# Kernel tuning notes

Hardware: AMD Instinct MI355X
Metric: run time of the kernel (lower is better)

Reference implementation:

```python
import jax, jax.numpy as jnp
import numpy as np

B, T, S, H = 32, 512, 1024, 512


def setup_inputs() -> dict:
    key = jax.random.key(0)
    k1, k2, k3, k4, k5, k6 = jax.random.split(key, 6)
    scale = 1.0 / np.sqrt(H)
    return {
        "query": jax.random.normal(k1, (B, T, H), dtype=jnp.float32),
        "encoder_outputs": jax.random.normal(k2, (B, S, H), dtype=jnp.float32),
        "src_lengths": jax.random.randint(k3, (B,), 1, S + 1, dtype=jnp.int32),
        "Ws": jax.random.normal(k4, (H, H), dtype=jnp.float32) * scale,  # torch Linear weight [out,in]
        "Wh": jax.random.normal(k5, (H, H), dtype=jnp.float32) * scale,
        "v": jax.random.normal(k6, (H,), dtype=jnp.float32) * scale,
    }


def reference(query, encoder_outputs, src_lengths, Ws, Wh, v):
    # score(h_s, q_t) = v^T tanh(Wh h_s + Ws q_t); masked softmax over src; weighted sum.
    S_ = encoder_outputs.shape[1]
    # Wh(encoder_outputs) computed once (loop in original recomputes it each step; same math).
    Whe = jnp.einsum('bsh,oh->bso', encoder_outputs, Wh)  # [B,S,H]
    mask = jnp.arange(S_)[None, :] < src_lengths[:, None]  # [B,S] valid positions

    def step(carry, q_t):  # q_t: [B,H]
        Wsq = jnp.einsum('bh,oh->bo', q_t, Ws)            # [B,H]
        scores = jnp.einsum('bsh,h->bs', jnp.tanh(Whe + Wsq[:, None, :]), v)  # [B,S]
        scores = jnp.where(mask, scores, -jnp.inf)
        attn = jax.nn.softmax(scores, axis=-1)            # [B,S]
        ctx = jnp.einsum('bs,bsh->bh', attn, encoder_outputs)  # [B,H]
        return carry, (ctx, attn)

    _, (ctx_t, attn_t) = jax.lax.scan(step, None, jnp.swapaxes(query, 0, 1))
    context_vectors = jnp.swapaxes(ctx_t, 0, 1)  # [B,T,H]
    # original returns attention weights from the LAST timestep only
    return context_vectors, attn_t[-1]
```

## Files before the change

### kernel.cpp

```cpp
#include <hip/hip_runtime.h>


constexpr int B = 32, T = 512, S = 1024, H = 512;
constexpr int TT = 16;
constexpr float C2LOG2E = 2.88539008177792681f;

typedef float vf4 __attribute__((ext_vector_type(4)));
typedef float f32x4 __attribute__((ext_vector_type(4)));
typedef short bf16x8 __attribute__((ext_vector_type(8)));
typedef unsigned short ushort_t;

#define DEVI __device__ __forceinline__

DEVI unsigned pack_bf16(float a, float b) {
  unsigned ua = __builtin_bit_cast(unsigned, a) + 0x8000u;
  unsigned ub = __builtin_bit_cast(unsigned, b) + 0x8000u;
  return (ub & 0xffff0000u) | (ua >> 16);
}
DEVI ushort_t to_bf16u(float x) {
  return (ushort_t)((__builtin_bit_cast(unsigned, x) + 0x8000u) >> 16);
}
DEVI float bf_lo(unsigned d) { return __builtin_bit_cast(float, d << 16); }
DEVI float bf_hi(unsigned d) { return __builtin_bit_cast(float, d & 0xffff0000u); }
DEVI float bf_one(ushort_t u) { return __builtin_bit_cast(float, (unsigned)u << 16); }
DEVI float exp2c(float x) {
  return __builtin_amdgcn_exp2f(fminf(fmaxf(x, -15.f), 15.f));
}

constexpr int QBLK = (B * T / 128) * 4;
constexpr int EBLK = (B * S / 128) * 4;

__global__ __launch_bounds__(256)
void mfma_matmul_kernel(const float* __restrict__ query, const float* __restrict__ enc,
                        const float* __restrict__ Ws, const float* __restrict__ Wh,
                        float* __restrict__ q4, float* __restrict__ e4,
                        const int* __restrict__ lens) {
  __shared__ short As[128][72];
  __shared__ short Bs[128][72];
  const int tid = threadIdx.x;
  int blk = blockIdx.x;
  const bool isE = blk >= QBLK;
  if (isE) blk -= QBLK;
  const int bx = blk & 3, by = blk >> 2;
  const int row0 = by * 128, col0 = bx * 128;
  const float* A = isE ? enc : query;
  const float* W = isE ? Wh : Ws;
  if (isE && (row0 % S) >= lens[row0 / S]) return;

  const int lr = tid >> 4;
  const int lc = (tid & 15) * 4;
  const int lane = tid & 63, wv = tid >> 6;
  const int wm = (wv >> 1) * 64, wn = (wv & 1) * 64;
  const int lrow = lane & 15, lkg = (lane >> 4) * 8;

  f32x4 acc[4][4] = {};
  for (int k0 = 0; k0 < H; k0 += 64) {
    __syncthreads();
#pragma unroll
    for (int u = 0; u < 8; ++u) {
      int r = lr + u * 16;
      float4 av = *(const float4*)&A[(size_t)(row0 + r) * H + k0 + lc];
      *(uint2*)&As[r][lc] = make_uint2(pack_bf16(av.x, av.y), pack_bf16(av.z, av.w));
      float4 wv4 = *(const float4*)&W[(size_t)(col0 + r) * H + k0 + lc];
      *(uint2*)&Bs[r][lc] = make_uint2(pack_bf16(wv4.x, wv4.y), pack_bf16(wv4.z, wv4.w));
    }
    __syncthreads();
#pragma unroll
    for (int ks = 0; ks < 64; ks += 32) {
      bf16x8 af[4], bfr[4];
#pragma unroll
      for (int i = 0; i < 4; ++i) {
        af[i] = *(const bf16x8*)&As[wm + i * 16 + lrow][ks + lkg];
        bfr[i] = *(const bf16x8*)&Bs[wn + i * 16 + lrow][ks + lkg];
      }
#pragma unroll
      for (int mt = 0; mt < 4; ++mt)
#pragma unroll
        for (int nt = 0; nt < 4; ++nt)
          acc[mt][nt] = __builtin_amdgcn_mfma_f32_16x16x32_bf16(
              af[mt], bfr[nt], acc[mt][nt], 0, 0, 0);
    }
  }

  const int crow = (lane >> 4) * 4, ccol = lane & 15;
  if (!isE) {
    const int b = row0 / T;
#pragma unroll
    for (int mt = 0; mt < 4; ++mt) {
      const int m = (row0 % T) + wm + mt * 16 + crow;
      const int tile_t = m >> 2;
#pragma unroll
      for (int nt = 0; nt < 4; ++nt) {
        const int n = col0 + wn + nt * 16 + ccol;
        float* base = q4 + (size_t)b * T * H + (size_t)tile_t * (4 * H) +
                      (n >> 2) * 16 + (n & 3);
        f32x4 a = acc[mt][nt];
#pragma unroll
        for (int reg = 0; reg < 4; ++reg) base[reg * 4] = exp2c(C2LOG2E * a[reg]);
      }
    }
  } else {
    const int b = row0 / S;
#pragma unroll
    for (int mt = 0; mt < 4; ++mt) {
      const int s0 = (row0 % S) + wm + mt * 16 + crow;
#pragma unroll
      for (int nt = 0; nt < 4; ++nt) {
        const int n = col0 + wn + nt * 16 + ccol;
        float* base = e4 + (size_t)b * H * S + (size_t)(n >> 2) * (4 * S) +
                      (size_t)s0 * 4 + (n & 3);
        f32x4 a = acc[mt][nt];
#pragma unroll
        for (int reg = 0; reg < 4; ++reg) base[reg * 4] = exp2c(C2LOG2E * a[reg]);
      }
    }
  }
}

DEVI void tree4(float& acc, vf4 q, vf4 vv, vf4 e) {
  float a0 = __builtin_fmaf(q[0], e[0], 1.0f);
  float a1 = __builtin_fmaf(q[1], e[1], 1.0f);
  float a2 = __builtin_fmaf(q[2], e[2], 1.0f);
  float a3 = __builtin_fmaf(q[3], e[3], 1.0f);
  float d01 = a0 * a1, d23 = a2 * a3;
  float n01 = __builtin_fmaf(vv[1], a0, vv[0] * a1);
  float n23 = __builtin_fmaf(vv[3], a2, vv[2] * a3);
  float d = d01 * d23;
  float n = __builtin_fmaf(n23, d01, n01 * d23);
  acc = __builtin_fmaf(n, __builtin_amdgcn_rcpf(d), acc);
}

DEVI vf4 qload(const ushort_t (&s_q16)[H / 4][64], int h4, int t) {
  uint2 qu = *(const uint2*)&s_q16[h4][t * 4];
  vf4 q = {bf_lo(qu.x), bf_hi(qu.x), bf_lo(qu.y), bf_hi(qu.y)};
  return q;
}

template <int NSIM>
DEVI void passN16(const ushort_t (&s_q16)[H / 4][64], const float* __restrict__ v,
                  const float* __restrict__ e4b, ushort_t (&s_sc16)[TT][S],
                  int wv, int lane) {
  float acc[NSIM][TT];
#pragma unroll
  for (int r = 0; r < NSIM; ++r)
#pragma unroll
    for (int t = 0; t < TT; ++t) acc[r][t] = 0.f;
  const float* ep = e4b + (size_t)(wv * 64 + lane) * 4;
  for (int h4 = 0; h4 < H / 4; ++h4) {
    vf4 e[NSIM];
#pragma unroll
    for (int r = 0; r < NSIM; ++r)
      e[r] = *(const vf4*)(ep + (size_t)h4 * (S * 4) + r * 1024);
    vf4 vv = *(const vf4*)(v + h4 * 4);
#pragma unroll
    for (int t = 0; t < TT; ++t) {
      vf4 q = qload(s_q16, h4, t);
#pragma unroll
      for (int r = 0; r < NSIM; ++r) tree4(acc[r][t], q, vv, e[r]);
    }
  }
#pragma unroll
  for (int r = 0; r < NSIM; ++r) {
    const int s = (wv + 4 * r) * 64 + lane;
#pragma unroll
    for (int t = 0; t < TT; ++t) s_sc16[t][s] = to_bf16u(-2.0f * acc[r][t]);
  }
}

template <int R>
DEVI void passTail16(const ushort_t (&s_q16)[H / 4][64], const float* __restrict__ v,
                     const float* __restrict__ e4b, ushort_t (&s_sc16)[TT][S],
                     int kbase, int wv, int lane) {
  float acc[R][4];
#pragma unroll
  for (int r = 0; r < R; ++r)
#pragma unroll
    for (int jj = 0; jj < 4; ++jj) acc[r][jj] = 0.f;
  const float* ep = e4b + (size_t)(kbase * 64 + lane) * 4;
  for (int h4 = 0; h4 < H / 4; ++h4) {
    vf4 vv = *(const vf4*)(v + h4 * 4);
    vf4 e[R];
#pragma unroll
    for (int r = 0; r < R; ++r)
      e[r] = *(const vf4*)(ep + (size_t)h4 * (S * 4) + r * 256);
#pragma unroll
    for (int jj = 0; jj < 4; ++jj) {
      vf4 q = qload(s_q16, h4, wv + 4 * jj);
#pragma unroll
      for (int r = 0; r < R; ++r) tree4(acc[r][jj], q, vv, e[r]);
    }
  }
#pragma unroll
  for (int r = 0; r < R; ++r)
#pragma unroll
    for (int jj = 0; jj < 4; ++jj)
      s_sc16[wv + 4 * jj][(kbase + r) * 64 + lane] = to_bf16u(-2.0f * acc[r][jj]);
}

__global__ __launch_bounds__(256, 3)
void attn_fused_kernel(const float* __restrict__ wsq, const float* __restrict__ wheT,
                       const float* __restrict__ enc, const float* __restrict__ v,
                       const int* __restrict__ lens, float* __restrict__ out) {
  __shared__ __align__(16) ushort_t s_sc16[TT][S];
  __shared__ __align__(16) ushort_t s_q16[H / 4][64];
  __shared__ float s_rs[TT];
  __shared__ long long s_w[32];
  __shared__ int s_bsel;

  const int tid = threadIdx.x;
  const int xcd = blockIdx.x & 7;
  const int j = blockIdx.x >> 3;
  const int slot = j >> 5;
  const int tt = j & 31;

  if (tid < 32) s_w[tid] = ((long long)lens[tid] << 8) + tid;
  __syncthreads();
  if (tid < 32) {
    long long wb = s_w[tid];
    int rank = 0;
#pragma unroll
    for (int b2 = 0; b2 < 32; ++b2) rank += (s_w[b2] > wb);
    int myrank = slot * 8 + ((slot & 1) ? (7 - xcd) : xcd);
    if (rank == myrank) s_bsel = tid;
  }
  __syncthreads();
  const int b = __builtin_amdgcn_readfirstlane(s_bsel);
  const int len = lens[b];

  {
    const vf4* src = (const vf4*)(wsq + (size_t)b * T * H + (size_t)tt * (TT * H));
    uint2* dst = (uint2*)&s_q16[0][0];
#pragma unroll
    for (int u = 0; u < 8; ++u) {
      int g = tid + u * 256;
      vf4 qv = src[g];
      int tile = g >> 9, rem = g & 511;
      int h4 = rem >> 2, i = rem & 3;
      uint2 pk = make_uint2(pack_bf16(qv[0], qv[1]), pack_bf16(qv[2], qv[3]));
      dst[h4 * 16 + tile * 4 + i] = pk;
    }
  }
  __syncthreads();

  {
    const int wv = tid >> 6, lane = tid & 63;
    const int NS = (len + 63) >> 6;
    const int nsw = NS >> 2;
    const int R = NS & 3;
    const float* e4b = wheT + (size_t)b * H * S;
    switch (nsw) {
      case 1: passN16<1>(s_q16, v, e4b, s_sc16, wv, lane); break;
      case 2: passN16<2>(s_q16, v, e4b, s_sc16, wv, lane); break;
      case 3: passN16<3>(s_q16, v, e4b, s_sc16, wv, lane); break;
      case 4: passN16<4>(s_q16, v, e4b, s_sc16, wv, lane); break;
      default: break;
    }
    switch (R) {
      case 1: passTail16<1>(s_q16, v, e4b, s_sc16, nsw * 4, wv, lane); break;
      case 2: passTail16<2>(s_q16, v, e4b, s_sc16, nsw * 4, wv, lane); break;
      case 3: passTail16<3>(s_q16, v, e4b, s_sc16, nsw * 4, wv, lane); break;
      default: break;
    }
  }
  __syncthreads();

  {
    const int wv = tid >> 6, lane = tid & 63;
#pragma unroll
    for (int jj = 0; jj < 4; ++jj) {
      const int tr = wv + 4 * jj;
      float vals[S / 64], ps[S / 64];
      float m = -3.0e38f;
#pragma unroll
      for (int i = 0; i < S / 64; ++i) {
        int s = lane + 64 * i;
        vals[i] = bf_one(s_sc16[tr][s]);
        if (s < len) m = fmaxf(m, vals[i]);
      }
#pragma unroll
      for (int o = 1; o < 64; o <<= 1) m = fmaxf(m, __shfl_xor(m, o, 64));
      float sum = 0.f;
#pragma unroll
      for (int i = 0; i < S / 64; ++i) {
        int s = lane + 64 * i;
        float p = (s < len) ? __builtin_amdgcn_exp2f((vals[i] - m) * 1.44269504088896341f) : 0.f;
        ps[i] = p;
        sum += p;
      }
#pragma unroll
      for (int o = 1; o < 64; o <<= 1) sum += __shfl_xor(sum, o, 64);
      float rs = 1.0f / sum;
#pragma unroll
      for (int i = 0; i < S / 64; ++i) s_sc16[tr][lane + 64 * i] = to_bf16u(ps[i]);
      if (lane == 0) s_rs[tr] = rs;
      if (tt == T / TT - 1 && tr == TT - 1) {
#pragma unroll
        for (int i = 0; i < S / 64; ++i)
          out[(size_t)B * T * H + (size_t)b * S + lane + 64 * i] = ps[i] * rs;
      }
    }
  }
  __syncthreads();

  {
    const int wv = tid >> 6, lane = tid & 63;
    const int h0 = lane * 4, h1 = 256 + lane * 4;
    float acc[4][8] = {};
    const float* encb = enc + (size_t)b * S * H;
    const int len4 = (len + 3) & ~3;
    for (int s0 = 0; s0 < len4; s0 += 4) {
      vf4 pr[4];
#pragma unroll
      for (int jj = 0; jj < 4; ++jj) {
        uint2 pu = *(const uint2*)&s_sc16[wv + 4 * jj][s0];
        pr[jj] = (vf4){bf_lo(pu.x), bf_hi(pu.x), bf_lo(pu.y), bf_hi(pu.y)};
      }
#pragma unroll
      for (int kk = 0; kk < 4; ++kk) {
        const float* er = encb + (size_t)(s0 + kk) * H;
        float4 e0 = *(const float4*)(er + h0);
        float4 e1 = *(const float4*)(er + h1);
        float ev[8] = {e0.x, e0.y, e0.z, e0.w, e1.x, e1.y, e1.z, e1.w};
#pragma unroll
        for (int jj = 0; jj < 4; ++jj)
#pragma unroll
          for (int q = 0; q < 8; ++q)
            acc[jj][q] = __builtin_fmaf(pr[jj][kk], ev[q], acc[jj][q]);
      }
    }
#pragma unroll
    for (int jj = 0; jj < 4; ++jj) {
      const int tr = wv + 4 * jj;
      const float rs = s_rs[tr];
      const size_t base = ((size_t)b * T + tt * TT + tr) * H;
      float4 o;
      o = make_float4(acc[jj][0] * rs, acc[jj][1] * rs, acc[jj][2] * rs, acc[jj][3] * rs);
      *(float4*)&out[base + h0] = o;
      o = make_float4(acc[jj][4] * rs, acc[jj][5] * rs, acc[jj][6] * rs, acc[jj][7] * rs);
      *(float4*)&out[base + h1] = o;
    }
  }
}

extern "C" void kernel_launch(void* const* d_in, const int* in_sizes, int n_in,
                              void* d_out, int out_size, void* d_ws, size_t ws_size,
                              hipStream_t stream) {
  const float* query = (const float*)d_in[0];
  const float* enc   = (const float*)d_in[1];
  const int*   lens  = (const int*)d_in[2];
  const float* Ws    = (const float*)d_in[3];
  const float* Wh    = (const float*)d_in[4];
  const float* v     = (const float*)d_in[5];
  float* out = (float*)d_out;
  float* wsq  = (float*)d_ws;
  float* wheT = wsq + (size_t)B * T * H;

  mfma_matmul_kernel<<<dim3(QBLK + EBLK), 256, 0, stream>>>(query, enc, Ws, Wh, wsq, wheT, lens);
  attn_fused_kernel<<<dim3(B * (T / TT)), 256, 0, stream>>>(wsq, wheT, enc, v, lens, out);
}
```

Before: 563.7 us.

## Stage bf16 query tile in quarters to shrink LDS and raise occupancy

Instead of converting the whole 16-timestep Wsq tile (512 hidden dims) into a 16 KB LDS buffer up front, the kernel now stages one quarter of the hidden dimension at a time into a 4 KB buffer inside the score passes, reloading from global for each quarter. This cuts LDS per block so more blocks can be resident, and launch bounds are raised from 3 to 4 waves-per-SIMD blocks. The cost is extra __syncthreads per quarter, re-staging the query for both main and tail passes, and tighter register limits that may cause spills for the larger NSIM variants.

```diff
diff --git a/kernel.cpp b/kernel.cpp
--- a/kernel.cpp
+++ b/kernel.cpp
@@ -130,33 +130,53 @@
   acc = __builtin_fmaf(n, __builtin_amdgcn_rcpf(d), acc);
 }
 
-DEVI vf4 qload(const ushort_t (&s_q16)[H / 4][64], int h4, int t) {
-  uint2 qu = *(const uint2*)&s_q16[h4][t * 4];
+DEVI vf4 qload4(const ushort_t (&s_q4)[32][64], int h4q, int t) {
+  uint2 qu = *(const uint2*)&s_q4[h4q][t * 4];
   vf4 q = {bf_lo(qu.x), bf_hi(qu.x), bf_lo(qu.y), bf_hi(qu.y)};
   return q;
 }
 
+DEVI void stage_quarter(ushort_t (&s_q4)[32][64], const vf4* __restrict__ qsrc,
+                        int qt, int tid) {
+  __syncthreads();
+#pragma unroll
+  for (int u = 0; u < 2; ++u) {
+    int g = tid + u * 256;
+    int tile = g >> 7, rem = g & 127;
+    int h4q = rem >> 2, i = rem & 3;
+    vf4 qv = qsrc[tile * 512 + (qt * 32 + h4q) * 4 + i];
+    uint2 pk = make_uint2(pack_bf16(qv[0], qv[1]), pack_bf16(qv[2], qv[3]));
+    ((uint2*)&s_q4[0][0])[h4q * 16 + tile * 4 + i] = pk;
+  }
+  __syncthreads();
+}
+
 template <int NSIM>
-DEVI void passN16(const ushort_t (&s_q16)[H / 4][64], const float* __restrict__ v,
-                  const float* __restrict__ e4b, ushort_t (&s_sc16)[TT][S],
-                  int wv, int lane) {
+DEVI void passN16(ushort_t (&s_q4)[32][64], const vf4* __restrict__ qsrc,
+                  const float* __restrict__ v, const float* __restrict__ e4b,
+                  ushort_t (&s_sc16)[TT][S], int wv, int lane) {
+  const int tid = wv * 64 + lane;
   float acc[NSIM][TT];
 #pragma unroll
   for (int r = 0; r < NSIM; ++r)
 #pragma unroll
     for (int t = 0; t < TT; ++t) acc[r][t] = 0.f;
   const float* ep = e4b + (size_t)(wv * 64 + lane) * 4;
-  for (int h4 = 0; h4 < H / 4; ++h4) {
-    vf4 e[NSIM];
-#pragma unroll
-    for (int r = 0; r < NSIM; ++r)
-      e[r] = *(const vf4*)(ep + (size_t)h4 * (S * 4) + r * 1024);
-    vf4 vv = *(const vf4*)(v + h4 * 4);
-#pragma unroll
-    for (int t = 0; t < TT; ++t) {
-      vf4 q = qload(s_q16, h4, t);
-#pragma unroll
-      for (int r = 0; r < NSIM; ++r) tree4(acc[r][t], q, vv, e[r]);
+  for (int qt = 0; qt < 4; ++qt) {
+    stage_quarter(s_q4, qsrc, qt, tid);
+    for (int h4q = 0; h4q < 32; ++h4q) {
+      const int h4 = qt * 32 + h4q;
+      vf4 e[NSIM];
+#pragma unroll
+      for (int r = 0; r < NSIM; ++r)
+        e[r] = *(const vf4*)(ep + (size_t)h4 * (S * 4) + r * 1024);
+      vf4 vv = *(const vf4*)(v + h4 * 4);
+#pragma unroll
+      for (int t = 0; t < TT; ++t) {
+        vf4 q = qload4(s_q4, h4q, t);
+#pragma unroll
+        for (int r = 0; r < NSIM; ++r) tree4(acc[r][t], q, vv, e[r]);
+      }
     }
   }
 #pragma unroll
@@ -168,26 +188,31 @@
 }
 
 template <int R>
-DEVI void passTail16(const ushort_t (&s_q16)[H / 4][64], const float* __restrict__ v,
-                     const float* __restrict__ e4b, ushort_t (&s_sc16)[TT][S],
-                     int kbase, int wv, int lane) {
+DEVI void passTail16(ushort_t (&s_q4)[32][64], const vf4* __restrict__ qsrc,
+                     const float* __restrict__ v, const float* __restrict__ e4b,
+                     ushort_t (&s_sc16)[TT][S], int kbase, int wv, int lane) {
+  const int tid = wv * 64 + lane;
   float acc[R][4];
 #pragma unroll
   for (int r = 0; r < R; ++r)
 #pragma unroll
     for (int jj = 0; jj < 4; ++jj) acc[r][jj] = 0.f;
   const float* ep = e4b + (size_t)(kbase * 64 + lane) * 4;
-  for (int h4 = 0; h4 < H / 4; ++h4) {
-    vf4 vv = *(const vf4*)(v + h4 * 4);
-    vf4 e[R];
-#pragma unroll
-    for (int r = 0; r < R; ++r)
-      e[r] = *(const vf4*)(ep + (size_t)h4 * (S * 4) + r * 256);
-#pragma unroll
-    for (int jj = 0; jj < 4; ++jj) {
-      vf4 q = qload(s_q16, h4, wv + 4 * jj);
-#pragma unroll
-      for (int r = 0; r < R; ++r) tree4(acc[r][jj], q, vv, e[r]);
+  for (int qt = 0; qt < 4; ++qt) {
+    stage_quarter(s_q4, qsrc, qt, tid);
+    for (int h4q = 0; h4q < 32; ++h4q) {
+      const int h4 = qt * 32 + h4q;
+      vf4 vv = *(const vf4*)(v + h4 * 4);
+      vf4 e[R];
+#pragma unroll
+      for (int r = 0; r < R; ++r)
+        e[r] = *(const vf4*)(ep + (size_t)h4 * (S * 4) + r * 256);
+#pragma unroll
+      for (int jj = 0; jj < 4; ++jj) {
+        vf4 q = qload4(s_q4, h4q, wv + 4 * jj);
+#pragma unroll
+        for (int r = 0; r < R; ++r) tree4(acc[r][jj], q, vv, e[r]);
+      }
     }
   }
 #pragma unroll
@@ -197,12 +222,12 @@
       s_sc16[wv + 4 * jj][(kbase + r) * 64 + lane] = to_bf16u(-2.0f * acc[r][jj]);
 }
 
-__global__ __launch_bounds__(256, 3)
+__global__ __launch_bounds__(256, 4)
 void attn_fused_kernel(const float* __restrict__ wsq, const float* __restrict__ wheT,
                        const float* __restrict__ enc, const float* __restrict__ v,
                        const int* __restrict__ lens, float* __restrict__ out) {
   __shared__ __align__(16) ushort_t s_sc16[TT][S];
-  __shared__ __align__(16) ushort_t s_q16[H / 4][64];
+  __shared__ __align__(16) ushort_t s_q4[32][64];
   __shared__ float s_rs[TT];
   __shared__ long long s_w[32];
   __shared__ int s_bsel;
@@ -226,21 +251,6 @@
   __syncthreads();
   const int b = __builtin_amdgcn_readfirstlane(s_bsel);
   const int len = lens[b];
-
-  {
-    const vf4* src = (const vf4*)(wsq + (size_t)b * T * H + (size_t)tt * (TT * H));
-    uint2* dst = (uint2*)&s_q16[0][0];
-#pragma unroll
-    for (int u = 0; u < 8; ++u) {
-      int g = tid + u * 256;
-      vf4 qv = src[g];
-      int tile = g >> 9, rem = g & 511;
-      int h4 = rem >> 2, i = rem & 3;
-      uint2 pk = make_uint2(pack_bf16(qv[0], qv[1]), pack_bf16(qv[2], qv[3]));
-      dst[h4 * 16 + tile * 4 + i] = pk;
-    }
-  }
-  __syncthreads();
 
   {
     const int wv = tid >> 6, lane = tid & 63;
@@ -248,17 +258,18 @@
     const int nsw = NS >> 2;
     const int R = NS & 3;
     const float* e4b = wheT + (size_t)b * H * S;
+    const vf4* qsrc = (const vf4*)(wsq + (size_t)b * T * H + (size_t)tt * (TT * H));
     switch (nsw) {
-      case 1: passN16<1>(s_q16, v, e4b, s_sc16, wv, lane); break;
-      case 2: passN16<2>(s_q16, v, e4b, s_sc16, wv, lane); break;
-      case 3: passN16<3>(s_q16, v, e4b, s_sc16, wv, lane); break;
-      case 4: passN16<4>(s_q16, v, e4b, s_sc16, wv, lane); break;
+      case 1: passN16<1>(s_q4, qsrc, v, e4b, s_sc16, wv, lane); break;
+      case 2: passN16<2>(s_q4, qsrc, v, e4b, s_sc16, wv, lane); break;
+      case 3: passN16<3>(s_q4, qsrc, v, e4b, s_sc16, wv, lane); break;
+      case 4: passN16<4>(s_q4, qsrc, v, e4b, s_sc16, wv, lane); break;
       default: break;
     }
     switch (R) {
-      case 1: passTail16<1>(s_q16, v, e4b, s_sc16, nsw * 4, wv, lane); break;
-      case 2: passTail16<2>(s_q16, v, e4b, s_sc16, nsw * 4, wv, lane); break;
-      case 3: passTail16<3>(s_q16, v, e4b, s_sc16, nsw * 4, wv, lane); break;
+      case 1: passTail16<1>(s_q4, qsrc, v, e4b, s_sc16, nsw * 4, wv, lane); break;
+      case 2: passTail16<2>(s_q4, qsrc, v, e4b, s_sc16, nsw * 4, wv, lane); break;
+      case 3: passTail16<3>(s_q4, qsrc, v, e4b, s_sc16, nsw * 4, wv, lane); break;
       default: break;
     }
   }
```

Result: no change. 560.5 us (-0.6%).
